# Performance work log

Hardware: AMD Instinct MI355X
Metric: run time of the kernel (lower is better)

The kernel has to match this reference:

```python
import jax, jax.numpy as jnp
import numpy as np

N = 100000      # nodes
E = 1600000     # edges
P = 262144      # pos/neg candidate edges
IN = 128        # in_channels
HID = 64        # hidden_channels
HEADS = 2
NEG_SLOPE = 0.2  # PyG GATConv default


def setup_inputs() -> dict:
    key = jax.random.key(0)
    ks = jax.random.split(key, 16)
    g = lambda k, shape, fan_in: jax.random.normal(k, shape, jnp.float32) * (1.0 / np.sqrt(fan_in))
    return {
        "x": jax.random.normal(ks[0], (N, IN), jnp.float32),
        "edge_index": jax.random.randint(ks[1], (2, E), 0, N),
        "edge_weight": jax.random.uniform(ks[2], (E,), jnp.float32),
        "pos_edge_index": jax.random.randint(ks[3], (2, P), 0, N),
        "neg_edge_index": jax.random.randint(ks[4], (2, P), 0, N),
        # conv1: in -> HEADS*HID
        "W1": g(ks[5], (IN, HEADS * HID), IN),
        "att_src1": g(ks[6], (HEADS, HID), HID),
        "att_dst1": g(ks[7], (HEADS, HID), HID),
        "b1": jnp.zeros((HEADS * HID,), jnp.float32),
        # conv2: HEADS*HID -> HID (heads=1)
        "W2": g(ks[8], (HEADS * HID, HID), HEADS * HID),
        "att_src2": g(ks[9], (1, HID), HID),
        "att_dst2": g(ks[10], (1, HID), HID),
        "b2": jnp.zeros((HID,), jnp.float32),
        # link_pred: Linear(2*HID, 1)
        "link_W": g(ks[11], (2 * HID, 1), 2 * HID),
        "link_b": jnp.zeros((1,), jnp.float32),
    }


def gat_layer(x, src, dst, W, a_src, a_dst, bias, heads, out_c, concat):
    n = x.shape[0]
    xw = (x @ W).reshape(n, heads, out_c)                      # [N, H, C]
    alpha_src = jnp.sum(xw * a_src, axis=-1)                   # [N, H]
    alpha_dst = jnp.sum(xw * a_dst, axis=-1)                   # [N, H]
    e = jax.nn.leaky_relu(alpha_src[src] + alpha_dst[dst], NEG_SLOPE)  # [E, H]
    # segment softmax over edges grouped by destination node
    m = jax.ops.segment_max(e, dst, num_segments=n)            # [N, H]
    ex = jnp.exp(e - m[dst])
    s = jax.ops.segment_sum(ex, dst, num_segments=n)
    alpha = ex / s[dst]                                        # [E, H]
    out = jax.ops.segment_sum(xw[src] * alpha[..., None], dst, num_segments=n)  # [N, H, C]
    out = out.reshape(n, heads * out_c) if concat else out.mean(axis=1)
    return out + bias


def reference(x, edge_index, edge_weight, pos_edge_index, neg_edge_index,
              W1, att_src1, att_dst1, b1, W2, att_src2, att_dst2, b2,
              link_W, link_b):
    n = x.shape[0]
    # PyG GATConv add_self_loops=True
    loop = jnp.arange(n)
    src = jnp.concatenate([edge_index[0], loop])
    dst = jnp.concatenate([edge_index[1], loop])

    h = gat_layer(x, src, dst, W1, att_src1, att_dst1, b1, HEADS, HID, True)
    h = jax.nn.relu(h)
    z = gat_layer(h, src, dst, W2, att_src2, att_dst2, b2, 1, HID, True)

    def decode(ei):
        feat = jnp.concatenate([z[ei[0]], z[ei[1]]], axis=1)   # [P, 2*HID]
        return (feat @ link_W + link_b).squeeze(-1)

    return decode(pos_edge_index), decode(neg_edge_index)
```

## Files before the change

kernel.cpp:

```cpp
#include <hip/hip_runtime.h>

#define N_NODES 100000
#define E_EDGES 1600000
#define EP      (E_EDGES + N_NODES)
#define P_CAND  262144
#define IN_C    128
#define HID     64
#define NEG_SLOPE 0.2f

#define NBIN  196
#define NB2   256
#define EPB   ((EP + NB2 - 1) / NB2)
#define NTOT  (NBIN * NB2)

typedef _Float16 half4v __attribute__((ext_vector_type(4)));
typedef _Float16 half8v __attribute__((ext_vector_type(8)));
typedef float    float4v __attribute__((ext_vector_type(4)));


__global__ __launch_bounds__(256) void hist_kernel(const int* __restrict__ ei,
                                                   int* __restrict__ hist) {
    __shared__ int lh[NBIN];
    for (int t = threadIdx.x; t < NBIN; t += 256) lh[t] = 0;
    __syncthreads();
    int start = blockIdx.x * EPB;
    int end = min(start + EPB, EP);
    for (int i = start + threadIdx.x; i < end; i += 256) {
        int dst = (i < E_EDGES) ? ei[E_EDGES + i] : (i - E_EDGES);
        atomicAdd(&lh[dst >> 9], 1);
    }
    __syncthreads();
    for (int t = threadIdx.x; t < NBIN; t += 256) hist[t * NB2 + blockIdx.x] = lh[t];
}

__global__ __launch_bounds__(1024) void scan2_kernel(const int* __restrict__ hist,
                                                     int* __restrict__ histS) {
    __shared__ int s[1024];
    int t = threadIdx.x;
    int b0 = t * 49;
    int sum = 0;
    for (int i = 0; i < 49; i++) sum += hist[b0 + i];
    s[t] = sum;
    __syncthreads();
    for (int d = 1; d < 1024; d <<= 1) {
        int v = (t >= d) ? s[t - d] : 0;
        __syncthreads();
        s[t] += v;
        __syncthreads();
    }
    int run = s[t] - sum;
    for (int i = 0; i < 49; i++) { int hv = hist[b0 + i]; histS[b0 + i] = run; run += hv; }
}

__global__ __launch_bounds__(256) void scatterbin_kernel(const int* __restrict__ ei,
                                                         const int* __restrict__ histS,
                                                         unsigned* __restrict__ binned) {
    __shared__ int cur[NBIN];
    for (int t = threadIdx.x; t < NBIN; t += 256) cur[t] = histS[t * NB2 + blockIdx.x];
    __syncthreads();
    int start = blockIdx.x * EPB;
    int end = min(start + EPB, EP);
    for (int i = start + threadIdx.x; i < end; i += 256) {
        int src, dst;
        if (i < E_EDGES) { src = ei[i]; dst = ei[E_EDGES + i]; }
        else             { src = i - E_EDGES; dst = src; }
        int pos = atomicAdd(&cur[dst >> 9], 1);
        binned[pos] = (unsigned)src | ((unsigned)(dst & 511) << 17);
    }
}

__global__ __launch_bounds__(1024) void binsort_kernel(const unsigned* __restrict__ binned,
                                                       const int* __restrict__ histS,
                                                       int* __restrict__ off,
                                                       int* __restrict__ csr) {
    __shared__ int lh[512];
    __shared__ int lsc[512];
    int b = blockIdx.x, t = threadIdx.x;
    int base = histS[b * NB2];
    int endv = (b == NBIN - 1) ? EP : histS[(b + 1) * NB2];
    if (t < 512) lh[t] = 0;
    __syncthreads();
    for (int i = base + t; i < endv; i += 1024)
        atomicAdd(&lh[binned[i] >> 17], 1);
    __syncthreads();
    if (t < 512) lsc[t] = lh[t];
    __syncthreads();
    for (int d = 1; d < 512; d <<= 1) {
        int v = (t >= d && t < 512) ? lsc[t - d] : 0;
        __syncthreads();
        if (t < 512) lsc[t] += v;
        __syncthreads();
    }
    if (t < 512) {
        int ex = lsc[t] - lh[t];
        int node = b * 512 + t;
        if (node <= N_NODES) off[node] = base + ex;
        lh[t] = base + ex;
    }
    __syncthreads();
    for (int i = base + t; i < endv; i += 1024) {
        unsigned v = binned[i];
        int pos = atomicAdd(&lh[v >> 17], 1);
        csr[pos] = (int)(v & 0x1FFFFu);
    }
}


__global__ __launch_bounds__(256) void prep_kernel(
        const float* __restrict__ W1, const float* __restrict__ W2,
        const float* __restrict__ att_src1, const float* __restrict__ att_dst1,
        const float* __restrict__ att_src2, const float* __restrict__ att_dst2,
        const float* __restrict__ b2, const float* __restrict__ lw,
        _Float16* __restrict__ W1T, _Float16* __restrict__ W2T,
        float* __restrict__ cvec) {
    int idx = blockIdx.x * 256 + threadIdx.x;
    if (idx < 16384) {
        int col = idx >> 7, k = idx & 127;
        W1T[idx] = (_Float16)W1[k * 128 + col];
    } else if (idx < 16896) {
        int j = idx - 16384;
        int c4 = j >> 7, k = j & 127;
        const float* av = (c4 < 2 ? att_src1 : att_dst1) + (c4 & 1) * 64;
        const float* wr = W1 + k * 128 + (c4 & 1) * 64;
        float s = 0.f;
        for (int c = 0; c < 64; c++) s += wr[c] * av[c];
        W1T[(128 + c4) * 128 + k] = (_Float16)s;
    } else if (idx < 18432) {
        W1T[132 * 128 + (idx - 16896)] = (_Float16)0.f;
    } else if (idx < 18944) {
        int j = idx - 18432;
        int c4 = j >> 7, k = j & 127;
        const float* av = (c4 == 0) ? att_src2 : (c4 == 1) ? att_dst2
                        : (c4 == 2) ? lw : (lw + 64);
        const float* wr = W2 + k * 64;
        float s = 0.f;
        for (int c = 0; c < 64; c++) s += wr[c] * av[c];
        W2T[c4 * 128 + k] = (_Float16)s;
    } else if (idx < 20480) {
        W2T[512 + (idx - 18944)] = (_Float16)0.f;
    } else if (idx < 20482) {
        int c = idx - 20480;
        const float* lwp = lw + c * 64;
        float s = 0.f;
        for (int i = 0; i < 64; i++) s += b2[i] * lwp[i];
        cvec[c] = s;
    }
}


__global__ __launch_bounds__(256) void gemm1_kernel(
        const float* __restrict__ x, const _Float16* __restrict__ W1T,
        unsigned char* __restrict__ xw1q, float* __restrict__ asp1,
        float* __restrict__ ad1) {
    __shared__ _Float16 xs[64 * 136];
    int tid = threadIdx.x;
    int base = blockIdx.x * 64;
    int w = tid >> 6, l = tid & 63;
    int quad = l >> 4, lq = l & 15;
    int row = base + 16 * w + lq;
    size_t rb = (size_t)(row < N_NODES ? row : 0) * 32;
    const float4* x4 = (const float4*)x;
    float4 af[8];
#pragma unroll
    for (int ks = 0; ks < 4; ks++) {
        af[2 * ks]     = x4[rb + ks * 8 + quad * 2];
        af[2 * ks + 1] = x4[rb + ks * 8 + quad * 2 + 1];
    }
    half8v a[4];
#pragma unroll
    for (int ks = 0; ks < 4; ks++) {
        float4 u0 = af[2 * ks], u1 = af[2 * ks + 1];
        half8v t;
        t[0] = (_Float16)u0.x; t[1] = (_Float16)u0.y; t[2] = (_Float16)u0.z; t[3] = (_Float16)u0.w;
        t[4] = (_Float16)u1.x; t[5] = (_Float16)u1.y; t[6] = (_Float16)u1.z; t[7] = (_Float16)u1.w;
        a[ks] = t;
    }
    float4v acc[9];
#pragma unroll
    for (int t = 0; t < 9; t++) acc[t] = (float4v)0.f;
#pragma unroll
    for (int ks = 0; ks < 4; ++ks) {
#pragma unroll
        for (int t = 0; t < 9; t++) {
            half8v b = *(const half8v*)&W1T[(t * 16 + lq) * 128 + ks * 32 + quad * 8];
            acc[t] = __builtin_amdgcn_mfma_f32_16x16x32_f16(a[ks], b, acc[t], 0, 0, 0);
        }
    }
    if (lq < 4) {
#pragma unroll
        for (int r = 0; r < 4; r++) {
            int n = base + 16 * w + quad * 4 + r;
            if (n < N_NODES) {
                if (lq < 2) asp1[4 * n + lq] = acc[8][r];
                else        ad1[2 * n + (lq & 1)] = acc[8][r];
            }
        }
    }
#pragma unroll
    for (int t = 0; t < 8; t++)
#pragma unroll
        for (int r = 0; r < 4; r++)
            xs[(16 * w + quad * 4 + r) * 136 + t * 16 + lq] = (_Float16)acc[t][r];
    __syncthreads();
    int node = tid >> 2, seg = tid & 3;
    if (base + node < N_NODES) {
        float vals[32];
        float mx = 0.f;
#pragma unroll
        for (int i = 0; i < 4; i++) {
            half8v vv = *(const half8v*)&xs[node * 136 + seg * 32 + i * 8];
#pragma unroll
            for (int k = 0; k < 8; k++) {
                float f = (float)vv[k];
                vals[i * 8 + k] = f;
                mx = fmaxf(mx, fabsf(f));
            }
        }
        mx = fmaxf(mx, __shfl_xor(mx, 1));
        mx = fmaxf(mx, __shfl_xor(mx, 2));
        mx = fmaxf(mx, 1e-20f);
        float r = 127.f / mx;
        unsigned pk[8];
#pragma unroll
        for (int d = 0; d < 8; d++) {
            unsigned u0 = (unsigned)(__float2int_rn(vals[d * 4 + 0] * r) + 128);
            unsigned u1 = (unsigned)(__float2int_rn(vals[d * 4 + 1] * r) + 128);
            unsigned u2 = (unsigned)(__float2int_rn(vals[d * 4 + 2] * r) + 128);
            unsigned u3 = (unsigned)(__float2int_rn(vals[d * 4 + 3] * r) + 128);
            pk[d] = u0 | (u1 << 8) | (u2 << 16) | (u3 << 24);
        }
        unsigned* dst = (unsigned*)&xw1q[(size_t)(base + node) * 128 + seg * 32];
        *(uint4*)dst       = make_uint4(pk[0], pk[1], pk[2], pk[3]);
        *(uint4*)(dst + 4) = make_uint4(pk[4], pk[5], pk[6], pk[7]);
        if (seg == 0) asp1[4 * (base + node) + 2] = mx * (1.f / 127.f);
    }
}


__global__ __launch_bounds__(256) void agg1_kernel(
        const int* __restrict__ off, const int* __restrict__ csr_src,
        const float* __restrict__ asp1, const float* __restrict__ ad1,
        const unsigned char* __restrict__ xw1q, const float* __restrict__ b1,
        _Float16* __restrict__ h) {
    __shared__ float2 esm[4][64];
    int wv = threadIdx.x >> 6, lane = threadIdx.x & 63;
    int ql = lane & 15;
    int gb = lane & 48;
    int n = blockIdx.x * 16 + (wv << 2) + (lane >> 4);
    int s = off[n], e = off[n + 1];
    float2 ad = *(const float2*)&ad1[2 * n];
    float adn0 = ad.x, adn1 = ad.y;
    const char* fl = (const char*)&esm[wv][gb] + ((ql >= 8) ? 4 : 0);
    const unsigned char* xq = xw1q + 8 * ql;
    float acc[8];
#pragma unroll
    for (int i = 0; i < 8; i++) acc[i] = 0.f;
    float sl0 = 0.f, sl1 = 0.f;
    float csum = 0.f;

#define DEQ1(QV, G) { \
    acc[0] = fmaf((float)((QV).x & 0xffu), (G), acc[0]); \
    acc[1] = fmaf((float)(((QV).x >> 8) & 0xffu), (G), acc[1]); \
    acc[2] = fmaf((float)(((QV).x >> 16) & 0xffu), (G), acc[2]); \
    acc[3] = fmaf((float)((QV).x >> 24), (G), acc[3]); \
    acc[4] = fmaf((float)((QV).y & 0xffu), (G), acc[4]); \
    acc[5] = fmaf((float)(((QV).y >> 8) & 0xffu), (G), acc[5]); \
    acc[6] = fmaf((float)(((QV).y >> 16) & 0xffu), (G), acc[6]); \
    acc[7] = fmaf((float)((QV).y >> 24), (G), acc[7]); }

    for (int b = s; b < e; b += 16) {
        int cnt = min(16, e - b);
        int l = ql < cnt ? ql : cnt - 1;
        int srcv = csr_src[b + l];
        float4 ap = *(const float4*)&asp1[4 * srcv];
        float e0 = ap.x + adn0; e0 = e0 > 0.f ? e0 : NEG_SLOPE * e0;
        float e1 = ap.y + adn1; e1 = e1 > 0.f ? e1 : NEG_SLOPE * e1;
        float f0v = (ql < cnt) ? __expf(e0) : 0.f;
        float f1v = (ql < cnt) ? __expf(e1) : 0.f;
        sl0 += f0v; sl1 += f1v;
        esm[wv][lane] = make_float2(f0v * ap.z, f1v * ap.z);
        int sj = __shfl(srcv, gb);
        uint2 qcur = *(const uint2*)&xq[(size_t)sj * 128];
        int j = 0;
        for (; j + 1 < cnt; ++j) {
            int sn = __shfl(srcv, gb + j + 1);
            uint2 qnxt = *(const uint2*)&xq[(size_t)sn * 128];
            float g = *(const float*)(fl + (size_t)j * 8);
            csum += g;
            DEQ1(qcur, g)
            qcur = qnxt;
        }
        { float g = *(const float*)(fl + (size_t)j * 8);
          csum += g; DEQ1(qcur, g) }
    }
#undef DEQ1
#pragma unroll
    for (int m = 8; m >= 1; m >>= 1) { sl0 += __shfl_xor(sl0, m); sl1 += __shfl_xor(sl1, m); }
    float sum = (ql >= 8) ? sl1 : sl0;
    float rs = __builtin_amdgcn_rcpf(sum);
    float base8 = -128.f * csum;
    int c = 8 * ql;
    half8v o;
#pragma unroll
    for (int i = 0; i < 8; i++) {
        float vv = fmaf(acc[i] + base8, rs, b1[c + i]);
        o[i] = (_Float16)(vv > 0.f ? vv : 0.f);
    }
    *(half8v*)&h[(size_t)n * 128 + c] = o;
}


__global__ __launch_bounds__(256) void gemm2_kernel(
        const _Float16* __restrict__ h, const _Float16* __restrict__ W2T,
        float* __restrict__ asp2) {
    int tid = threadIdx.x;
    int base = blockIdx.x * 64;
    int w = tid >> 6, l = tid & 63;
    int quad = l >> 4, lq = l & 15;
    int row = base + 16 * w + lq;
    size_t rbase = (size_t)(row < N_NODES ? row : 0) * 128;
    half8v a[4];
#pragma unroll
    for (int ks = 0; ks < 4; ks++)
        a[ks] = *(const half8v*)&h[rbase + ks * 32 + quad * 8];
    float4v acc = (float4v)0.f;
#pragma unroll
    for (int ks = 0; ks < 4; ++ks) {
        half8v b = *(const half8v*)&W2T[lq * 128 + ks * 32 + quad * 8];
        acc = __builtin_amdgcn_mfma_f32_16x16x32_f16(a[ks], b, acc, 0, 0, 0);
    }
    if (lq < 4) {
        int slot = (lq == 0) ? 0 : (lq == 1) ? 3 : (lq == 2) ? 1 : 2;
#pragma unroll
        for (int r = 0; r < 4; r++) {
            int n = base + 16 * w + quad * 4 + r;
            if (n < N_NODES) asp2[4 * n + slot] = acc[r];
        }
    }
}


__global__ __launch_bounds__(256) void agg2_kernel(
        const int* __restrict__ off, const int* __restrict__ csr_src,
        const float* __restrict__ asp2, const float* __restrict__ cvec,
        float* __restrict__ u, float* __restrict__ v) {
    int wv = threadIdx.x >> 6, lane = threadIdx.x & 63;
    int ql = lane & 15;
    int n = blockIdx.x * 16 + (wv << 2) + (lane >> 4);
    int s = off[n], e = off[n + 1];
    float adn = asp2[4 * n + 3];
    float sf = 0.f, s1 = 0.f, s2 = 0.f;
    for (int j = s + ql; j < e; j += 16) {
        int srcv = csr_src[j];
        float4 ap = *(const float4*)&asp2[4 * srcv];
        float ev = ap.x + adn; ev = ev > 0.f ? ev : NEG_SLOPE * ev;
        float f = __expf(ev);
        sf += f;
        s1 = fmaf(f, ap.y, s1);
        s2 = fmaf(f, ap.z, s2);
    }
#pragma unroll
    for (int m = 8; m >= 1; m >>= 1) {
        sf += __shfl_xor(sf, m);
        s1 += __shfl_xor(s1, m);
        s2 += __shfl_xor(s2, m);
    }
    if (ql == 0) {
        float rs = __builtin_amdgcn_rcpf(sf);
        u[n] = fmaf(s1, rs, cvec[0]);
        v[n] = fmaf(s2, rs, cvec[1]);
    }
}


__global__ __launch_bounds__(256) void decode_kernel(
        const int* __restrict__ pos_ei, const int* __restrict__ neg_ei,
        const float* __restrict__ u, const float* __restrict__ v,
        const float* __restrict__ lb, float* __restrict__ out) {
    int idx = blockIdx.x * 256 + threadIdx.x;
    if (idx >= 2 * P_CAND) return;
    const int* ei; int p;
    if (idx < P_CAND) { ei = pos_ei; p = idx; }
    else              { ei = neg_ei; p = idx - P_CAND; }
    int sN = ei[p], dN = ei[P_CAND + p];
    out[idx] = u[sN] + v[dN] + lb[0];
}


extern "C" void kernel_launch(void* const* d_in, const int* in_sizes, int n_in,
                              void* d_out, int out_size, void* d_ws, size_t ws_size,
                              hipStream_t stream) {
    const float* x        = (const float*)d_in[0];
    const int*   ei       = (const int*)d_in[1];
    const int*   pos_ei   = (const int*)d_in[3];
    const int*   neg_ei   = (const int*)d_in[4];
    const float* W1       = (const float*)d_in[5];
    const float* att_src1 = (const float*)d_in[6];
    const float* att_dst1 = (const float*)d_in[7];
    const float* b1       = (const float*)d_in[8];
    const float* W2       = (const float*)d_in[9];
    const float* att_src2 = (const float*)d_in[10];
    const float* att_dst2 = (const float*)d_in[11];
    const float* b2       = (const float*)d_in[12];
    const float* lw       = (const float*)d_in[13];
    const float* lb       = (const float*)d_in[14];
    float* out = (float*)d_out;

    char* ws = (char*)d_ws;
    size_t o = 0;
    auto alloc = [&](size_t bytes) -> char* {
        char* p = ws + o;
        o += (bytes + 511) & ~(size_t)511;
        return p;
    };
    unsigned char* xw1q = (unsigned char*)alloc((size_t)N_NODES * 128);
    float*    asp1  = (float*)alloc((size_t)N_NODES * 4 * 4);
    float*    ad1   = (float*)alloc((size_t)N_NODES * 2 * 4);
    _Float16* h     = (_Float16*)alloc((size_t)N_NODES * 128 * 2 + 16384);
    float*    asp2  = (float*)alloc((size_t)N_NODES * 4 * 4);
    float*    cvec  = (float*)alloc(512);
    float*    u     = (float*)alloc((size_t)N_NODES * 4);
    float*    v     = (float*)alloc((size_t)N_NODES * 4);
    int*      off   = (int*)alloc((size_t)(N_NODES + 1) * 4);
    int*      hist  = (int*)alloc((size_t)NTOT * 4);
    int*      histS = (int*)alloc((size_t)NTOT * 4);
    unsigned* binned= (unsigned*)alloc((size_t)EP * 4);
    int*      csr   = (int*)alloc((size_t)EP * 4);
    _Float16* W1T   = (_Float16*)alloc((size_t)144 * 128 * 2);
    _Float16* W2T   = (_Float16*)alloc((size_t)16 * 128 * 2);

    prep_kernel<<<81, 256, 0, stream>>>(W1, W2, att_src1, att_dst1, att_src2, att_dst2,
                                        b2, lw, W1T, W2T, cvec);
    hist_kernel<<<NB2, 256, 0, stream>>>(ei, hist);
    scan2_kernel<<<1, 1024, 0, stream>>>(hist, histS);
    scatterbin_kernel<<<NB2, 256, 0, stream>>>(ei, histS, binned);
    binsort_kernel<<<NBIN, 1024, 0, stream>>>(binned, histS, off, csr);
    gemm1_kernel<<<(N_NODES + 63) / 64, 256, 0, stream>>>(x, W1T, xw1q, asp1, ad1);
    agg1_kernel<<<N_NODES / 16, 256, 0, stream>>>(off, csr, asp1, ad1, xw1q, b1, h);
    gemm2_kernel<<<(N_NODES + 63) / 64, 256, 0, stream>>>(h, W2T, asp2);
    agg2_kernel<<<N_NODES / 16, 256, 0, stream>>>(off, csr, asp2, cvec, u, v);
    decode_kernel<<<(2 * P_CAND + 255) / 256, 256, 0, stream>>>(pos_ei, neg_ei, u, v, lb, out);
}
```

Baseline: 289.1 us.

## Split single-block histogram scan into per-bin wave scans plus bin-offset scan

Replaces the single 1024-thread scan kernel, which walks 49 serial entries per thread, with a 196-block kernel that scans each bin's 256 per-block counts using wavefront shuffles, followed by a tiny kernel that scans the bin totals. The scatter kernel now adds the bin offset to the row scan, and binsort reads bin bounds from the new offset array. Binsort's 512-entry shared-memory Hillis-Steele scan is also replaced by wave shuffle scans plus an 8-entry wave prefix. This removes a serial single-block bottleneck and many barriers, at the cost of one extra kernel launch.

```diff
diff --git a/kernel.cpp b/kernel.cpp
--- a/kernel.cpp
+++ b/kernel.cpp
@@ -33,30 +33,53 @@
     for (int t = threadIdx.x; t < NBIN; t += 256) hist[t * NB2 + blockIdx.x] = lh[t];
 }
 
-__global__ __launch_bounds__(1024) void scan2_kernel(const int* __restrict__ hist,
-                                                     int* __restrict__ histS) {
-    __shared__ int s[1024];
-    int t = threadIdx.x;
-    int b0 = t * 49;
-    int sum = 0;
-    for (int i = 0; i < 49; i++) sum += hist[b0 + i];
-    s[t] = sum;
-    __syncthreads();
-    for (int d = 1; d < 1024; d <<= 1) {
-        int v = (t >= d) ? s[t - d] : 0;
+__global__ __launch_bounds__(256) void scanA_kernel(const int* __restrict__ hist,
+                                                    int* __restrict__ rowscan,
+                                                    int* __restrict__ binsum) {
+    int t = blockIdx.x;
+    int c = threadIdx.x;
+    int v = hist[t * NB2 + c];
+    int lane = c & 63, w = c >> 6;
+    int iv = v;
+#pragma unroll
+    for (int d = 1; d < 64; d <<= 1) {
+        int o = __shfl_up(iv, d);
+        if (lane >= d) iv += o;
+    }
+    __shared__ int wt[4];
+    if (lane == 63) wt[w] = iv;
+    __syncthreads();
+    int add = 0;
+    for (int i = 0; i < w; i++) add += wt[i];
+    int inc = iv + add;
+    rowscan[t * NB2 + c] = inc - v;
+    if (c == 255) binsum[t] = inc;
+}
+
+__global__ __launch_bounds__(256) void scanB_kernel(const int* __restrict__ binsum,
+                                                    int* __restrict__ binoff) {
+    __shared__ int s[256];
+    int c = threadIdx.x;
+    int v = (c < NBIN) ? binsum[c] : 0;
+    s[c] = v;
+    __syncthreads();
+    for (int d = 1; d < 256; d <<= 1) {
+        int o = (c >= d) ? s[c - d] : 0;
         __syncthreads();
-        s[t] += v;
+        s[c] += o;
         __syncthreads();
     }
-    int run = s[t] - sum;
-    for (int i = 0; i < 49; i++) { int hv = hist[b0 + i]; histS[b0 + i] = run; run += hv; }
+    if (c == 0) binoff[0] = 0;
+    if (c < NBIN) binoff[c + 1] = s[c];
 }
 
 __global__ __launch_bounds__(256) void scatterbin_kernel(const int* __restrict__ ei,
-                                                         const int* __restrict__ histS,
+                                                         const int* __restrict__ rowscan,
+                                                         const int* __restrict__ binoff,
                                                          unsigned* __restrict__ binned) {
     __shared__ int cur[NBIN];
-    for (int t = threadIdx.x; t < NBIN; t += 256) cur[t] = histS[t * NB2 + blockIdx.x];
+    for (int t = threadIdx.x; t < NBIN; t += 256)
+        cur[t] = binoff[t] + rowscan[t * NB2 + blockIdx.x];
     __syncthreads();
     int start = blockIdx.x * EPB;
     int end = min(start + EPB, EP);
@@ -70,29 +93,37 @@
 }
 
 __global__ __launch_bounds__(1024) void binsort_kernel(const unsigned* __restrict__ binned,
-                                                       const int* __restrict__ histS,
+                                                       const int* __restrict__ binoff,
                                                        int* __restrict__ off,
                                                        int* __restrict__ csr) {
     __shared__ int lh[512];
-    __shared__ int lsc[512];
+    __shared__ int wpre[8];
     int b = blockIdx.x, t = threadIdx.x;
-    int base = histS[b * NB2];
-    int endv = (b == NBIN - 1) ? EP : histS[(b + 1) * NB2];
+    int base = binoff[b];
+    int endv = binoff[b + 1];
     if (t < 512) lh[t] = 0;
     __syncthreads();
     for (int i = base + t; i < endv; i += 1024)
         atomicAdd(&lh[binned[i] >> 17], 1);
     __syncthreads();
-    if (t < 512) lsc[t] = lh[t];
-    __syncthreads();
-    for (int d = 1; d < 512; d <<= 1) {
-        int v = (t >= d && t < 512) ? lsc[t - d] : 0;
-        __syncthreads();
-        if (t < 512) lsc[t] += v;
-        __syncthreads();
-    }
+    int iv = 0, lane = t & 63, w = t >> 6;
     if (t < 512) {
-        int ex = lsc[t] - lh[t];
+        iv = lh[t];
+#pragma unroll
+        for (int d = 1; d < 64; d <<= 1) {
+            int o = __shfl_up(iv, d);
+            if (lane >= d) iv += o;
+        }
+        if (lane == 63) wpre[w] = iv;
+    }
+    __syncthreads();
+    if (t == 0) {
+        int run = 0;
+        for (int i = 0; i < 8; i++) { int x = wpre[i]; wpre[i] = run; run += x; }
+    }
+    __syncthreads();
+    if (t < 512) {
+        int ex = iv + wpre[w] - lh[t];
         int node = b * 512 + t;
         if (node <= N_NODES) off[node] = base + ex;
         lh[t] = base + ex;
@@ -423,7 +454,9 @@
     float*    v     = (float*)alloc((size_t)N_NODES * 4);
     int*      off   = (int*)alloc((size_t)(N_NODES + 1) * 4);
     int*      hist  = (int*)alloc((size_t)NTOT * 4);
-    int*      histS = (int*)alloc((size_t)NTOT * 4);
+    int*      rowscan = (int*)alloc((size_t)NTOT * 4);
+    int*      binsum  = (int*)alloc(256 * 4);
+    int*      binoff  = (int*)alloc(256 * 4);
     unsigned* binned= (unsigned*)alloc((size_t)EP * 4);
     int*      csr   = (int*)alloc((size_t)EP * 4);
     _Float16* W1T   = (_Float16*)alloc((size_t)144 * 128 * 2);
@@ -432,9 +465,10 @@
     prep_kernel<<<81, 256, 0, stream>>>(W1, W2, att_src1, att_dst1, att_src2, att_dst2,
                                         b2, lw, W1T, W2T, cvec);
     hist_kernel<<<NB2, 256, 0, stream>>>(ei, hist);
-    scan2_kernel<<<1, 1024, 0, stream>>>(hist, histS);
-    scatterbin_kernel<<<NB2, 256, 0, stream>>>(ei, histS, binned);
-    binsort_kernel<<<NBIN, 1024, 0, stream>>>(binned, histS, off, csr);
+    scanA_kernel<<<NBIN, 256, 0, stream>>>(hist, rowscan, binsum);
+    scanB_kernel<<<1, 256, 0, stream>>>(binsum, binoff);
+    scatterbin_kernel<<<NB2, 256, 0, stream>>>(ei, rowscan, binoff, binned);
+    binsort_kernel<<<NBIN, 1024, 0, stream>>>(binned, binoff, off, csr);
     gemm1_kernel<<<(N_NODES + 63) / 64, 256, 0, stream>>>(x, W1T, xw1q, asp1, ad1);
     agg1_kernel<<<N_NODES / 16, 256, 0, stream>>>(off, csr, asp1, ad1, xw1q, b1, h);
     gemm2_kernel<<<(N_NODES + 63) / 64, 256, 0, stream>>>(h, W2T, asp2);
```

Result: faster. 270.8 us (-6.3%).
